# Optimization experiments

Measured on AMD Instinct MI355X. Metric: run time of the kernel, lower is better.

The kernel has to match this reference:

```python
import jax, jax.numpy as jnp
import numpy as np

B, T, D = 2, 2048, 2048
NH, NKV, HD = 16, 4, 128
ROPE_DIMS = 64
EPS = 1e-6


def _rope_tables(t, rd, base=10000.0):
    # rd dims are rotated as two halves of size rd//2; cos/sin are [T, rd]
    inv_freq = 1.0 / (base ** (jnp.arange(0, rd // 2, dtype=jnp.float32) * 2.0 / rd))
    ang = jnp.arange(t, dtype=jnp.float32)[:, None] * inv_freq[None, :]  # [T, rd//2]
    ang = jnp.concatenate([ang, ang], axis=-1)  # [T, rd]
    return jnp.cos(ang), jnp.sin(ang)


def setup_inputs() -> dict:
    key = jax.random.key(0)
    ks = jax.random.split(key, 6)
    x = jax.random.normal(ks[0], (B, T, D), dtype=jnp.float32)
    cos, sin = _rope_tables(T, ROPE_DIMS)
    s = 1.0 / np.sqrt(D)
    wq = jax.random.normal(ks[1], (NH * HD, D), dtype=jnp.float32) * s
    wk = jax.random.normal(ks[2], (NKV * HD, D), dtype=jnp.float32) * s
    wv = jax.random.normal(ks[3], (NKV * HD, D), dtype=jnp.float32) * s
    wo = jax.random.normal(ks[4], (NH * HD, D), dtype=jnp.float32).T * s  # [NH*HD, D] -> stored torch-style below
    wo = jax.random.normal(ks[5], (D, NH * HD), dtype=jnp.float32) * s  # torch Linear weight [out,in]
    w_norm = jnp.ones((D,), dtype=jnp.float32)
    return {"x": x, "cos": cos, "sin": sin, "w_norm": w_norm, "wq": wq,
            "wk": wk, "wv": wv, "wo": wo, "rope_dims": ROPE_DIMS, "use_xsa": 1}


def _rmsnorm(x, w, eps=EPS):
    ms = jnp.mean(x * x, axis=-1, keepdims=True)
    return x * jax.lax.rsqrt(ms + eps) * w


def _rotate_half(x):
    x1, x2 = jnp.split(x, 2, axis=-1)
    return jnp.concatenate([-x2, x1], axis=-1)


def _apply_partial_rope(q, k, cos, sin, rd):
    # q: [B,T,NH,HD], k: [B,T,NKV,HD]; cos/sin: [T,rd]
    c = cos[None, :, None, :]
    s = sin[None, :, None, :]
    def rot(t):
        tr, tp = t[..., :rd], t[..., rd:]
        tr = tr * c + _rotate_half(tr) * s
        return jnp.concatenate([tr, tp], axis=-1)
    return rot(q), rot(k)


def reference(x, cos, sin, w_norm, wq, wk, wv, wo, rope_dims, use_xsa):
    b, t, d = x.shape
    group = NH // NKV
    h = _rmsnorm(x, w_norm)
    q = jnp.einsum('btd,ed->bte', h, wq).reshape(b, t, NH, HD)
    k = jnp.einsum('btd,ed->bte', h, wk).reshape(b, t, NKV, HD)
    v = jnp.einsum('btd,ed->bte', h, wv).reshape(b, t, NKV, HD)
    q, k = _apply_partial_rope(q, k, cos, sin, rope_dims)
    # GQA: repeat KV heads across groups, then [B,H,T,HD]
    k = jnp.repeat(k, group, axis=2).transpose(0, 2, 1, 3)
    v = jnp.repeat(v, group, axis=2).transpose(0, 2, 1, 3)
    q = q.transpose(0, 2, 1, 3)
    scores = jnp.einsum('bhqd,bhkd->bhqk', q, k) / np.sqrt(HD)
    causal = jnp.tril(jnp.ones((t, t), dtype=bool))
    scores = jnp.where(causal[None, None], scores, jnp.finfo(scores.dtype).min)
    attn = jax.nn.softmax(scores, axis=-1)
    out = jnp.einsum('bhqk,bhkd->bhqd', attn, v)
    if use_xsa:
        dot = jnp.sum(out * v, axis=-1, keepdims=True)
        vns = jnp.sum(v * v, axis=-1, keepdims=True) + 1e-6
        out = out - dot * v / vns
    out = out.transpose(0, 2, 1, 3).reshape(b, t, NH * HD)
    return jnp.einsum('bte,de->btd', out, wo)
```

## Files before the change

### kernel.cpp

```cpp
#include <hip/hip_runtime.h>
#include <hip/hip_bf16.h>
#include <stdint.h>

#define B_ 2
#define T_ 2048
#define D_ 2048
#define NH_ 16
#define NKV_ 4
#define HD_ 128
#define EQ_ (NH_*HD_)
#define EKV_ (NKV_*HD_)
#define EQKV_ (EQ_ + 2*EKV_)
#define KOFF_ EQ_
#define VOFF_ (EQ_ + EKV_)

typedef __attribute__((ext_vector_type(8))) short short8;
typedef __attribute__((ext_vector_type(4))) short short4x;
typedef __attribute__((ext_vector_type(4))) float floatx4;

static __device__ __forceinline__ ushort f2bf(float f) {
  uint u = __builtin_bit_cast(uint, f);
  u = (u + 0x7fffu + ((u >> 16) & 1u)) >> 16;
  return (ushort)u;
}
static __device__ __forceinline__ float bf2f(ushort u) {
  return __builtin_bit_cast(float, ((uint)u) << 16);
}

#define S1_ (EQ_*D_)
#define S2_ (S1_ + EKV_*D_)
#define S3_ (S2_ + EKV_*D_)
#define S4_ (S3_ + D_*EQ_)
__global__ __launch_bounds__(256) void cvt4_k(const float* __restrict__ wq,
                                              const float* __restrict__ wk,
                                              const float* __restrict__ wv,
                                              const float* __restrict__ wo,
                                              ushort* __restrict__ wqkv,
                                              ushort* __restrict__ wob) {
  int i = (blockIdx.x * 256 + threadIdx.x) * 2;
  const float* s;
  ushort* d;
  int j;
  if (i < S1_)      { s = wq; d = wqkv + i; j = i; }
  else if (i < S2_) { s = wk; d = wqkv + i; j = i - S1_; }
  else if (i < S3_) { s = wv; d = wqkv + i; j = i - S2_; }
  else              { s = wo; d = wob + (i - S3_); j = i - S3_; }
  float2 f = *(const float2*)&s[j];
  ushort2 u;
  u.x = f2bf(f.x);
  u.y = f2bf(f.y);
  *(ushort2*)d = u;
}

__global__ __launch_bounds__(256) void rmsnorm_k(const float* __restrict__ x,
                                                 const float* __restrict__ wn,
                                                 ushort* __restrict__ hb) {
  const int row = blockIdx.x, tid = threadIdx.x;
  const int w = tid >> 6, lane = tid & 63;
  const float* xr = x + (size_t)row * D_;
  float v[8];
  float4 a = *(const float4*)&xr[tid * 8];
  float4 b = *(const float4*)&xr[tid * 8 + 4];
  v[0] = a.x; v[1] = a.y; v[2] = a.z; v[3] = a.w;
  v[4] = b.x; v[5] = b.y; v[6] = b.z; v[7] = b.w;
  float ss = 0.f;
#pragma unroll
  for (int i = 0; i < 8; i++) ss += v[i] * v[i];
  for (int m = 32; m; m >>= 1) ss += __shfl_xor(ss, m);
  __shared__ float red[4];
  if (lane == 0) red[w] = ss;
  __syncthreads();
  float tot = red[0] + red[1] + red[2] + red[3];
  float sc = rsqrtf(tot * (1.f / D_) + 1e-6f);
  short8 st;
#pragma unroll
  for (int i = 0; i < 8; i++) st[i] = (short)f2bf(v[i] * sc * wn[tid * 8 + i]);
  *(short8*)(hb + (size_t)row * D_ + tid * 8) = st;
}

template <bool OUT_F32>
__global__ __launch_bounds__(256) void gemm_bt(const ushort* __restrict__ A,
                                               const ushort* __restrict__ W,
                                               void* __restrict__ Cp,
                                               int M, int N, int K) {
  __shared__ __align__(16) ushort lA[128 * 64];
  __shared__ __align__(16) ushort lB[128 * 64];
  const int tid = threadIdx.x;
  const int w = tid >> 6, lane = tid & 63;
  const int bm = blockIdx.y, bn = blockIdx.x;
  const int wm = w >> 1, wn = w & 1;
  const int l15 = lane & 15, l4 = lane >> 4;
  const int swz = (l15 & 7) * 8;

  floatx4 acc[4][4];
#pragma unroll
  for (int m = 0; m < 4; m++)
#pragma unroll
    for (int n = 0; n < 4; n++) acc[m][n] = floatx4{0.f, 0.f, 0.f, 0.f};

  for (int k0 = 0; k0 < K; k0 += 64) {
#pragma unroll
    for (int r = 0; r < 4; ++r) {
      int c = r * 256 + tid;
      int row = c >> 3, cw = c & 7;
      int scol = k0 + ((cw ^ (row & 7)) << 3);
      const ushort* ga = A + (size_t)(bm * 128 + row) * K + scol;
      __builtin_amdgcn_global_load_lds(
          (const __attribute__((address_space(1))) void*)ga,
          (__attribute__((address_space(3))) void*)&lA[c * 8], 16, 0, 0);
      const ushort* gb = W + (size_t)(bn * 128 + row) * K + scol;
      __builtin_amdgcn_global_load_lds(
          (const __attribute__((address_space(1))) void*)gb,
          (__attribute__((address_space(3))) void*)&lB[c * 8], 16, 0, 0);
    }
    __syncthreads();
#pragma unroll
    for (int kk = 0; kk < 2; kk++) {
      short8 av[4], bv[4];
      int co = (kk * 32 + l4 * 8) ^ swz;
#pragma unroll
      for (int m = 0; m < 4; m++)
        av[m] = *(const short8*)&lA[(wm * 64 + m * 16 + l15) * 64 + co];
#pragma unroll
      for (int n = 0; n < 4; n++)
        bv[n] = *(const short8*)&lB[(wn * 64 + n * 16 + l15) * 64 + co];
#pragma unroll
      for (int m = 0; m < 4; m++)
#pragma unroll
        for (int n = 0; n < 4; n++)
          acc[m][n] = __builtin_amdgcn_mfma_f32_16x16x32_bf16(av[m], bv[n], acc[m][n], 0, 0, 0);
    }
    __syncthreads();
  }

  if (OUT_F32) {
    float* C = (float*)Cp;
#pragma unroll
    for (int m = 0; m < 4; m++)
#pragma unroll
      for (int n = 0; n < 4; n++)
#pragma unroll
        for (int j = 0; j < 4; j++) {
          int row = bm * 128 + wm * 64 + m * 16 + l4 * 4 + j;
          int col = bn * 128 + wn * 64 + n * 16 + l15;
          C[(size_t)row * N + col] = acc[m][n][j];
        }
  } else {
    ushort* C = (ushort*)Cp;
#pragma unroll
    for (int m = 0; m < 4; m++)
#pragma unroll
      for (int n = 0; n < 4; n++)
#pragma unroll
        for (int j = 0; j < 4; j++) {
          int row = bm * 128 + wm * 64 + m * 16 + l4 * 4 + j;
          int col = bn * 128 + wn * 64 + n * 16 + l15;
          C[(size_t)row * N + col] = f2bf(acc[m][n][j]);
        }
  }
}

__global__ __launch_bounds__(256) void rope_k(ushort* __restrict__ X,
                                              const float* __restrict__ cosT,
                                              const float* __restrict__ sinT,
                                              int rd) {
  int idx = blockIdx.x * 256 + threadIdx.x;
  int half = rd >> 1;
  int total = B_ * T_ * (NH_ + NKV_) * half;
  if (idx >= total) return;
  int i = idx % half;
  int r2 = idx / half;
  int hh = r2 % (NH_ + NKV_);
  int row = r2 / (NH_ + NKV_);
  int t = row % T_;
  int col = (hh < NH_) ? hh * HD_ : KOFF_ + (hh - NH_) * HD_;
  ushort* p = X + (size_t)row * EQKV_ + col;
  float x0 = bf2f(p[i]), x1 = bf2f(p[i + half]);
  float c0 = cosT[t * rd + i], s0 = sinT[t * rd + i];
  float c1 = cosT[t * rd + i + half], s1 = sinT[t * rd + i + half];
  p[i] = f2bf(x0 * c0 - x1 * s0);
  p[i + half] = f2bf(x1 * c1 + x0 * s1);
}

__global__ __launch_bounds__(256) void vtr_k(const ushort* __restrict__ V,
                                             int vstride,
                                             ushort* __restrict__ Vt) {
  __shared__ ushort tile[32][34];
  const int tb = blockIdx.x, eb = blockIdx.y, b = blockIdx.z;
  const int tid = threadIdx.x;
  const int r = tid >> 3, c4 = (tid & 7) * 4;
  short4x in = *(const short4x*)&V[((size_t)(b * T_ + tb * 32 + r)) * vstride + eb * 32 + c4];
#pragma unroll
  for (int i = 0; i < 4; i++) tile[r][c4 + i] = (ushort)in[i];
  __syncthreads();
  short4x out;
#pragma unroll
  for (int i = 0; i < 4; i++) out[i] = (short)tile[c4 + i][r];
  *(short4x*)&Vt[((size_t)(b * EKV_ + eb * 32 + r)) * T_ + tb * 32 + c4] = out;
}

__global__ __launch_bounds__(256, 2) void attn_k(const ushort* __restrict__ QKV,
                                                 const ushort* __restrict__ Vt,
                                                 const int* __restrict__ flag,
                                                 ushort* __restrict__ att) {
  __shared__ __align__(16) ushort Klds[2][8192];
  __shared__ __align__(16) ushort Vlds[2][8192];
  __shared__ __align__(16) char P_lds[4 * 2048];
  const int tid = threadIdx.x, w = tid >> 6, lane = tid & 63;
  const int l15 = lane & 15, l4 = lane >> 4;
  const int h = blockIdx.y, b = blockIdx.z, kv = h >> 2;
  const int px = blockIdx.x;
  const int wbase = w * 2048;
  const float c_ = 0.12752626f;
  const float THR_ = 90.5f;
  const int flagv = *flag;

  const ushort* Kh = QKV + KOFF_ + (size_t)b * T_ * EQKV_ + kv * HD_;
  const ushort* Vth = Vt + ((size_t)(b * EKV_ + kv * HD_)) * T_;

  auto stageK = [&](int buf, const ushort* kp) {
#pragma unroll
    for (int i = 0; i < 4; i++) {
      int q = i * 256 + tid;
      int r = q >> 4, cw = q & 15;
      const ushort* src = kp + (size_t)r * EQKV_ + ((cw ^ (r & 7)) << 3);
      __builtin_amdgcn_global_load_lds(
          (const __attribute__((address_space(1))) void*)src,
          (__attribute__((address_space(3))) void*)&Klds[buf][q * 8], 16, 0, 0);
    }
  };
  auto stageV = [&](int buf, const ushort* vp) {
#pragma unroll
    for (int i = 0; i < 4; i++) {
      int q = i * 256 + tid;
      int d = q >> 3, cw = q & 7;
      const ushort* src = vp + (size_t)d * T_ + ((cw ^ (d & 7)) << 3);
      __builtin_amdgcn_global_load_lds(
          (const __attribute__((address_space(1))) void*)src,
          (__attribute__((address_space(3))) void*)&Vlds[buf][q * 8], 16, 0, 0);
    }
  };

  for (int hh = 0; hh < 2; hh++) {
    const int qb = hh ? (31 - px) : px;
    const int nt = qb + 1;
    const int qbase = qb * 64 + w * 16;

    short8 qf[4];
#pragma unroll
    for (int kk = 0; kk < 4; kk++)
      qf[kk] = *(const short8*)&QKV[(size_t)(b * T_ + qbase + l15) * EQKV_ + h * HD_ + kk * 32 + l4 * 8];

    floatx4 acc_o[8];
#pragma unroll
    for (int nn = 0; nn < 8; nn++) acc_o[nn] = floatx4{0.f, 0.f, 0.f, 0.f};
    float mj[4] = {-1e30f, -1e30f, -1e30f, -1e30f};
    float lj[4] = {0.f, 0.f, 0.f, 0.f};

    const ushort* kp = Kh;
    const ushort* vp = Vth;
    stageV(0, vp);
    stageK(0, kp);
    __syncthreads();
    int cur = 0;

    for (int t = 0; t < nt; t++) {
      if (t + 1 < nt) {
        stageV(cur ^ 1, vp + 64);
        stageK(cur ^ 1, kp + 64 * EQKV_);
      }
      kp += 64 * EQKV_;
      vp += 64;

      floatx4 s[4];
#pragma unroll
      for (int n = 0; n < 4; n++) s[n] = floatx4{0.f, 0.f, 0.f, 0.f};
      __builtin_amdgcn_s_setprio(1);
#pragma unroll
      for (int n = 0; n < 4; n++) {
        int row = n * 16 + l15;
#pragma unroll
        for (int kk = 0; kk < 4; kk++) {
          int bc = (kk * 64 + l4 * 16) ^ ((row & 7) << 4);
          short8 kf = *(const short8*)&Klds[cur][row * 128 + (bc >> 1)];
          s[n] = __builtin_amdgcn_mfma_f32_16x16x32_bf16(qf[kk], kf, s[n], 0, 0, 0);
        }
      }
      __builtin_amdgcn_s_setprio(0);

      float pm[4] = {-1e30f, -1e30f, -1e30f, -1e30f};
      if (t == nt - 1) {
#pragma unroll
        for (int n = 0; n < 4; n++)
#pragma unroll
          for (int j = 0; j < 4; j++) {
            int col = (nt - 1) * 64 + n * 16 + l15;
            int row = qbase + l4 * 4 + j;
            float sv = (col <= row) ? s[n][j] : -1e30f;
            s[n][j] = sv;
            pm[j] = fmaxf(pm[j], sv);
          }
      } else {
#pragma unroll
        for (int n = 0; n < 4; n++)
#pragma unroll
          for (int j = 0; j < 4; j++) pm[j] = fmaxf(pm[j], s[n][j]);
      }
#pragma unroll
      for (int j = 0; j < 4; j++) {
        pm[j] = fmaxf(pm[j], __shfl_xor(pm[j], 1));
        pm[j] = fmaxf(pm[j], __shfl_xor(pm[j], 2));
        pm[j] = fmaxf(pm[j], __shfl_xor(pm[j], 4));
        pm[j] = fmaxf(pm[j], __shfl_xor(pm[j], 8));
      }
      float worst = fmaxf(fmaxf(pm[0] - mj[0], pm[1] - mj[1]),
                          fmaxf(pm[2] - mj[2], pm[3] - mj[3]));
      if (!__all(worst <= THR_)) {
#pragma unroll
        for (int j = 0; j < 4; j++) {
          float mn = fmaxf(mj[j], pm[j]);
          float sc = exp2f((mj[j] - mn) * c_);
          mj[j] = mn;
          lj[j] *= sc;
#pragma unroll
          for (int nn = 0; nn < 8; nn++) acc_o[nn][j] *= sc;
        }
      }
      float mc[4];
#pragma unroll
      for (int j = 0; j < 4; j++) mc[j] = mj[j] * c_;
      float ps[4] = {0.f, 0.f, 0.f, 0.f};
#pragma unroll
      for (int n = 0; n < 4; n++)
#pragma unroll
        for (int j = 0; j < 4; j++) {
          float p = exp2f(__builtin_fmaf(s[n][j], c_, -mc[j]));
          ps[j] += p;
          uint pu = (__builtin_bit_cast(uint, p) + 0x8000u) >> 16;
          int r = l4 * 4 + j;
          int byteoff = ((r * 128 + (n * 16 + l15) * 2) ^ ((r & 7) << 4));
          *(ushort*)(P_lds + wbase + byteoff) = (ushort)pu;
        }

      __builtin_amdgcn_s_setprio(1);
#pragma unroll
      for (int kk = 0; kk < 2; kk++) {
        int rbyte = ((l15 * 128 + kk * 64 + l4 * 16) ^ ((l15 & 7) << 4));
        short8 pa = *(const short8*)(P_lds + wbase + rbyte);
#pragma unroll
        for (int n = 0; n < 8; n++) {
          int d = n * 16 + l15;
          int bc = (kk * 64 + l4 * 16) ^ ((d & 7) << 4);
          short8 vf = *(const short8*)&Vlds[cur][d * 64 + (bc >> 1)];
          acc_o[n] = __builtin_amdgcn_mfma_f32_16x16x32_bf16(pa, vf, acc_o[n], 0, 0, 0);
        }
      }
      __builtin_amdgcn_s_setprio(0);
#pragma unroll
      for (int j = 0; j < 4; j++) {
        ps[j] += __shfl_xor(ps[j], 1);
        ps[j] += __shfl_xor(ps[j], 2);
        ps[j] += __shfl_xor(ps[j], 4);
        ps[j] += __shfl_xor(ps[j], 8);
        lj[j] += ps[j];
      }
      __syncthreads();
      cur ^= 1;
    }

#pragma unroll
    for (int j = 0; j < 4; j++) {
      float inv = 1.f / lj[j];
      int q = qbase + l4 * 4 + j;
      const ushort* vq = QKV + VOFF_ + (size_t)(b * T_ + q) * EQKV_ + kv * HD_;
      float ov[8], vv[8], dot = 0.f, vns = 0.f;
#pragma unroll
      for (int n = 0; n < 8; n++) {
        float o = acc_o[n][j] * inv;
        float v = bf2f(vq[n * 16 + l15]);
        ov[n] = o;
        vv[n] = v;
        dot += o * v;
        vns += v * v;
      }
      dot += __shfl_xor(dot, 1); vns += __shfl_xor(vns, 1);
      dot += __shfl_xor(dot, 2); vns += __shfl_xor(vns, 2);
      dot += __shfl_xor(dot, 4); vns += __shfl_xor(vns, 4);
      dot += __shfl_xor(dot, 8); vns += __shfl_xor(vns, 8);
      if (flagv) {
        float f = dot / (vns + 1e-6f);
#pragma unroll
        for (int n = 0; n < 8; n++) ov[n] -= f * vv[n];
      }
      ushort* ap = att + (size_t)(b * T_ + q) * EQ_ + h * HD_;
#pragma unroll
      for (int n = 0; n < 8; n++) ap[n * 16 + l15] = f2bf(ov[n]);
    }
  }
}

extern "C" void kernel_launch(void* const* d_in, const int* in_sizes, int n_in,
                              void* d_out, int out_size, void* d_ws, size_t ws_size,
                              hipStream_t stream) {
  const float* x    = (const float*)d_in[0];
  const float* cosT = (const float*)d_in[1];
  const float* sinT = (const float*)d_in[2];
  const float* wn   = (const float*)d_in[3];
  const float* wq   = (const float*)d_in[4];
  const float* wk   = (const float*)d_in[5];
  const float* wv   = (const float*)d_in[6];
  const float* wo   = (const float*)d_in[7];
  const int* use_xsa = (const int*)d_in[9];
  int rd = in_sizes[1] / T_;

  char* ws = (char*)d_ws;
  size_t off = 0;
  auto alloc = [&](size_t bytes) {
    char* p = ws + off;
    off += (bytes + 255) & ~(size_t)255;
    return p;
  };
  ushort* h_b    = (ushort*)alloc((size_t)B_ * T_ * D_ * 2);
  ushort* qkv_b  = (ushort*)alloc((size_t)B_ * T_ * EQKV_ * 2);
  ushort* wqkv_b = (ushort*)alloc((size_t)EQKV_ * D_ * 2);
  ushort* wo_b   = (ushort*)alloc((size_t)D_ * EQ_ * 2);
  ushort* att_b  = h_b;
  ushort* vt_b   = wqkv_b;

  cvt4_k<<<S4_ / 512, 256, 0, stream>>>(wq, wk, wv, wo, wqkv_b, wo_b);
  rmsnorm_k<<<B_ * T_, 256, 0, stream>>>(x, wn, h_b);

  dim3 gqkv(EQKV_ / 128, B_ * T_ / 128);
  gemm_bt<false><<<gqkv, 256, 0, stream>>>(h_b, wqkv_b, qkv_b, B_ * T_, EQKV_, D_);

  dim3 gvt(T_ / 32, EKV_ / 32, B_);
  vtr_k<<<gvt, 256, 0, stream>>>(qkv_b + VOFF_, EQKV_, vt_b);

  int half = rd / 2;
  int tot = B_ * T_ * (NH_ + NKV_) * half;
  rope_k<<<(tot + 255) / 256, 256, 0, stream>>>(qkv_b, cosT, sinT, rd);

  dim3 ga(16, NH_, B_);
  attn_k<<<ga, 256, 0, stream>>>(qkv_b, vt_b, use_xsa, att_b);

  dim3 go(D_ / 128, B_ * T_ / 128);
  gemm_bt<true><<<go, 256, 0, stream>>>(att_b, wo_b, d_out, B_ * T_, D_, D_);
}
```

Measured before the change: 225.1 us.

## Load V fragments directly from global memory and raise attention occupancy

The attention kernel no longer stages transposed V tiles into double-buffered LDS. Each wave now reads its V fragments straight from global memory (via cache) inside the PV loop, and the launch bound is raised from 2 to 4 blocks per CU. Dropping the V buffers cuts LDS use so more blocks can fit on a CU, trading shared staging for redundant per-wave global loads with latency exposed right before the MFMAs. The tighter register budget from the higher launch bound may force spills.

```diff
diff --git a/kernel.cpp b/kernel.cpp
--- a/kernel.cpp
+++ b/kernel.cpp
@@ -199,12 +199,11 @@
   *(short4x*)&Vt[((size_t)(b * EKV_ + eb * 32 + r)) * T_ + tb * 32 + c4] = out;
 }
 
-__global__ __launch_bounds__(256, 2) void attn_k(const ushort* __restrict__ QKV,
+__global__ __launch_bounds__(256, 4) void attn_k(const ushort* __restrict__ QKV,
                                                  const ushort* __restrict__ Vt,
                                                  const int* __restrict__ flag,
                                                  ushort* __restrict__ att) {
   __shared__ __align__(16) ushort Klds[2][8192];
-  __shared__ __align__(16) ushort Vlds[2][8192];
   __shared__ __align__(16) char P_lds[4 * 2048];
   const int tid = threadIdx.x, w = tid >> 6, lane = tid & 63;
   const int l15 = lane & 15, l4 = lane >> 4;
@@ -229,17 +228,6 @@
           (__attribute__((address_space(3))) void*)&Klds[buf][q * 8], 16, 0, 0);
     }
   };
-  auto stageV = [&](int buf, const ushort* vp) {
-#pragma unroll
-    for (int i = 0; i < 4; i++) {
-      int q = i * 256 + tid;
-      int d = q >> 3, cw = q & 7;
-      const ushort* src = vp + (size_t)d * T_ + ((cw ^ (d & 7)) << 3);
-      __builtin_amdgcn_global_load_lds(
-          (const __attribute__((address_space(1))) void*)src,
-          (__attribute__((address_space(3))) void*)&Vlds[buf][q * 8], 16, 0, 0);
-    }
-  };
 
   for (int hh = 0; hh < 2; hh++) {
     const int qb = hh ? (31 - px) : px;
@@ -258,19 +246,15 @@
     float lj[4] = {0.f, 0.f, 0.f, 0.f};
 
     const ushort* kp = Kh;
-    const ushort* vp = Vth;
-    stageV(0, vp);
     stageK(0, kp);
     __syncthreads();
     int cur = 0;
 
     for (int t = 0; t < nt; t++) {
-      if (t + 1 < nt) {
-        stageV(cur ^ 1, vp + 64);
+      const int kvb = t * 64;
+      if (t + 1 < nt)
         stageK(cur ^ 1, kp + 64 * EQKV_);
-      }
       kp += 64 * EQKV_;
-      vp += 64;
 
       floatx4 s[4];
 #pragma unroll
@@ -345,15 +329,15 @@
       __builtin_amdgcn_s_setprio(1);
 #pragma unroll
       for (int kk = 0; kk < 2; kk++) {
+        short8 vf[8];
+#pragma unroll
+        for (int n = 0; n < 8; n++)
+          vf[n] = *(const short8*)&Vth[(size_t)(n * 16 + l15) * T_ + kvb + kk * 32 + l4 * 8];
         int rbyte = ((l15 * 128 + kk * 64 + l4 * 16) ^ ((l15 & 7) << 4));
         short8 pa = *(const short8*)(P_lds + wbase + rbyte);
 #pragma unroll
-        for (int n = 0; n < 8; n++) {
-          int d = n * 16 + l15;
-          int bc = (kk * 64 + l4 * 16) ^ ((d & 7) << 4);
-          short8 vf = *(const short8*)&Vlds[cur][d * 64 + (bc >> 1)];
-          acc_o[n] = __builtin_amdgcn_mfma_f32_16x16x32_bf16(pa, vf, acc_o[n], 0, 0, 0);
-        }
+        for (int n = 0; n < 8; n++)
+          acc_o[n] = __builtin_amdgcn_mfma_f32_16x16x32_bf16(pa, vf[n], acc_o[n], 0, 0, 0);
       }
       __builtin_amdgcn_s_setprio(0);
 #pragma unroll
```

Result: slower. 353.8 us (+57.2%).

## Compute transposed S tile and feed P to PV MFMA via lane shuffles

Applied to the files above, without the earlier changes.

Swaps the QK^T MFMA operands so each lane holds scores for a single query row. Row max and sum then need only two cross-lane shuffles instead of sixteen, and online-softmax state becomes one scalar per lane. P is packed to bf16 with v_cvt_pk_bf16_f32 and rearranged into the PV A-operand layout with ds_bpermute shuffles, which removes the P staging buffer in LDS and its write/read round trip. In exchange it adds per-tile shuffles for the rescale factors and the P fragments, plus select logic.

```diff
diff --git a/kernel.cpp b/kernel.cpp
--- a/kernel.cpp
+++ b/kernel.cpp
@@ -17,6 +17,7 @@
 typedef __attribute__((ext_vector_type(8))) short short8;
 typedef __attribute__((ext_vector_type(4))) short short4x;
 typedef __attribute__((ext_vector_type(4))) float floatx4;
+typedef __attribute__((ext_vector_type(4))) uint uintx4;
 
 static __device__ __forceinline__ ushort f2bf(float f) {
   uint u = __builtin_bit_cast(uint, f);
@@ -25,6 +26,11 @@
 }
 static __device__ __forceinline__ float bf2f(ushort u) {
   return __builtin_bit_cast(float, ((uint)u) << 16);
+}
+static __device__ __forceinline__ uint cvt_pk_bf16(float lo, float hi) {
+  uint r;
+  asm("v_cvt_pk_bf16_f32 %0, %1, %2" : "=v"(r) : "v"(lo), "v"(hi));
+  return r;
 }
 
 #define S1_ (EQ_*D_)
@@ -205,12 +211,13 @@
                                                  ushort* __restrict__ att) {
   __shared__ __align__(16) ushort Klds[2][8192];
   __shared__ __align__(16) ushort Vlds[2][8192];
-  __shared__ __align__(16) char P_lds[4 * 2048];
   const int tid = threadIdx.x, w = tid >> 6, lane = tid & 63;
   const int l15 = lane & 15, l4 = lane >> 4;
+  const int alpha = lane >> 5;
+  const int srcA = ((lane >> 4) & 1) * 32 + l15;
+  const int srcB = srcA + 16;
   const int h = blockIdx.y, b = blockIdx.z, kv = h >> 2;
   const int px = blockIdx.x;
-  const int wbase = w * 2048;
   const float c_ = 0.12752626f;
   const float THR_ = 90.5f;
   const int flagv = *flag;
@@ -245,6 +252,7 @@
     const int qb = hh ? (31 - px) : px;
     const int nt = qb + 1;
     const int qbase = qb * 64 + w * 16;
+    const int myq = qbase + l15;
 
     short8 qf[4];
 #pragma unroll
@@ -254,8 +262,8 @@
     floatx4 acc_o[8];
 #pragma unroll
     for (int nn = 0; nn < 8; nn++) acc_o[nn] = floatx4{0.f, 0.f, 0.f, 0.f};
-    float mj[4] = {-1e30f, -1e30f, -1e30f, -1e30f};
-    float lj[4] = {0.f, 0.f, 0.f, 0.f};
+    float m_ = -1e30f;
+    float l_ = 0.f;
 
     const ushort* kp = Kh;
     const ushort* vp = Vth;
@@ -265,6 +273,7 @@
     int cur = 0;
 
     for (int t = 0; t < nt; t++) {
+      const int kvb = t * 64;
       if (t + 1 < nt) {
         stageV(cur ^ 1, vp + 64);
         stageK(cur ^ 1, kp + 64 * EQKV_);
@@ -283,70 +292,87 @@
         for (int kk = 0; kk < 4; kk++) {
           int bc = (kk * 64 + l4 * 16) ^ ((row & 7) << 4);
           short8 kf = *(const short8*)&Klds[cur][row * 128 + (bc >> 1)];
-          s[n] = __builtin_amdgcn_mfma_f32_16x16x32_bf16(qf[kk], kf, s[n], 0, 0, 0);
+          s[n] = __builtin_amdgcn_mfma_f32_16x16x32_bf16(kf, qf[kk], s[n], 0, 0, 0);
         }
       }
       __builtin_amdgcn_s_setprio(0);
 
-      float pm[4] = {-1e30f, -1e30f, -1e30f, -1e30f};
+      float pm = -1e30f;
       if (t == nt - 1) {
 #pragma unroll
         for (int n = 0; n < 4; n++)
 #pragma unroll
           for (int j = 0; j < 4; j++) {
-            int col = (nt - 1) * 64 + n * 16 + l15;
-            int row = qbase + l4 * 4 + j;
-            float sv = (col <= row) ? s[n][j] : -1e30f;
+            int k = kvb + n * 16 + l4 * 4 + j;
+            float sv = (k <= myq) ? s[n][j] : -1e30f;
             s[n][j] = sv;
-            pm[j] = fmaxf(pm[j], sv);
+            pm = fmaxf(pm, sv);
           }
       } else {
 #pragma unroll
         for (int n = 0; n < 4; n++)
 #pragma unroll
-          for (int j = 0; j < 4; j++) pm[j] = fmaxf(pm[j], s[n][j]);
-      }
-#pragma unroll
-      for (int j = 0; j < 4; j++) {
-        pm[j] = fmaxf(pm[j], __shfl_xor(pm[j], 1));
-        pm[j] = fmaxf(pm[j], __shfl_xor(pm[j], 2));
-        pm[j] = fmaxf(pm[j], __shfl_xor(pm[j], 4));
-        pm[j] = fmaxf(pm[j], __shfl_xor(pm[j], 8));
-      }
-      float worst = fmaxf(fmaxf(pm[0] - mj[0], pm[1] - mj[1]),
-                          fmaxf(pm[2] - mj[2], pm[3] - mj[3]));
-      if (!__all(worst <= THR_)) {
+          for (int j = 0; j < 4; j++) pm = fmaxf(pm, s[n][j]);
+      }
+      pm = fmaxf(pm, __shfl_xor(pm, 16));
+      pm = fmaxf(pm, __shfl_xor(pm, 32));
+
+      if (!__all(pm - m_ <= THR_)) {
+        float mn = fmaxf(m_, pm);
+        float f = exp2f((m_ - mn) * c_);
+        m_ = mn;
+        l_ *= f;
+        float fj0 = __shfl(f, l4 * 4 + 0);
+        float fj1 = __shfl(f, l4 * 4 + 1);
+        float fj2 = __shfl(f, l4 * 4 + 2);
+        float fj3 = __shfl(f, l4 * 4 + 3);
+#pragma unroll
+        for (int nn = 0; nn < 8; nn++) {
+          acc_o[nn][0] *= fj0;
+          acc_o[nn][1] *= fj1;
+          acc_o[nn][2] *= fj2;
+          acc_o[nn][3] *= fj3;
+        }
+      }
+
+      float mc = m_ * c_;
+      float ps = 0.f;
+      float p_[4][4];
+#pragma unroll
+      for (int n = 0; n < 4; n++)
 #pragma unroll
         for (int j = 0; j < 4; j++) {
-          float mn = fmaxf(mj[j], pm[j]);
-          float sc = exp2f((mj[j] - mn) * c_);
-          mj[j] = mn;
-          lj[j] *= sc;
-#pragma unroll
-          for (int nn = 0; nn < 8; nn++) acc_o[nn][j] *= sc;
-        }
-      }
-      float mc[4];
-#pragma unroll
-      for (int j = 0; j < 4; j++) mc[j] = mj[j] * c_;
-      float ps[4] = {0.f, 0.f, 0.f, 0.f};
-#pragma unroll
-      for (int n = 0; n < 4; n++)
-#pragma unroll
-        for (int j = 0; j < 4; j++) {
-          float p = exp2f(__builtin_fmaf(s[n][j], c_, -mc[j]));
-          ps[j] += p;
-          uint pu = (__builtin_bit_cast(uint, p) + 0x8000u) >> 16;
-          int r = l4 * 4 + j;
-          int byteoff = ((r * 128 + (n * 16 + l15) * 2) ^ ((r & 7) << 4));
-          *(ushort*)(P_lds + wbase + byteoff) = (ushort)pu;
-        }
+          float p = exp2f(__builtin_fmaf(s[n][j], c_, -mc));
+          p_[n][j] = p;
+          ps += p;
+        }
+      ps += __shfl_xor(ps, 16);
+      ps += __shfl_xor(ps, 32);
+      l_ += ps;
+      uint pk01[4], pk23[4];
+#pragma unroll
+      for (int n = 0; n < 4; n++) {
+        pk01[n] = cvt_pk_bf16(p_[n][0], p_[n][1]);
+        pk23[n] = cvt_pk_bf16(p_[n][2], p_[n][3]);
+      }
 
       __builtin_amdgcn_s_setprio(1);
 #pragma unroll
       for (int kk = 0; kk < 2; kk++) {
-        int rbyte = ((l15 * 128 + kk * 64 + l4 * 16) ^ ((l15 & 7) << 4));
-        short8 pa = *(const short8*)(P_lds + wbase + rbyte);
+        int a01_0 = __shfl((int)pk01[2 * kk + 0], srcA);
+        int a01_1 = __shfl((int)pk01[2 * kk + 1], srcA);
+        int a23_0 = __shfl((int)pk23[2 * kk + 0], srcA);
+        int a23_1 = __shfl((int)pk23[2 * kk + 1], srcA);
+        int b01_0 = __shfl((int)pk01[2 * kk + 0], srcB);
+        int b01_1 = __shfl((int)pk01[2 * kk + 1], srcB);
+        int b23_0 = __shfl((int)pk23[2 * kk + 0], srcB);
+        int b23_1 = __shfl((int)pk23[2 * kk + 1], srcB);
+        uintx4 du;
+        du.x = (uint)(alpha ? a01_1 : a01_0);
+        du.y = (uint)(alpha ? a23_1 : a23_0);
+        du.z = (uint)(alpha ? b01_1 : b01_0);
+        du.w = (uint)(alpha ? b23_1 : b23_0);
+        short8 pa = __builtin_bit_cast(short8, du);
 #pragma unroll
         for (int n = 0; n < 8; n++) {
           int d = n * 16 + l15;
@@ -356,21 +382,14 @@
         }
       }
       __builtin_amdgcn_s_setprio(0);
-#pragma unroll
-      for (int j = 0; j < 4; j++) {
-        ps[j] += __shfl_xor(ps[j], 1);
-        ps[j] += __shfl_xor(ps[j], 2);
-        ps[j] += __shfl_xor(ps[j], 4);
-        ps[j] += __shfl_xor(ps[j], 8);
-        lj[j] += ps[j];
-      }
       __syncthreads();
       cur ^= 1;
     }
 
+    float inv_ = 1.f / l_;
 #pragma unroll
     for (int j = 0; j < 4; j++) {
-      float inv = 1.f / lj[j];
+      float inv = __shfl(inv_, l4 * 4 + j);
       int q = qbase + l4 * 4 + j;
       const ushort* vq = QKV + VOFF_ + (size_t)(b * T_ + q) * EQKV_ + kv * HD_;
       float ov[8], vv[8], dot = 0.f, vns = 0.f;
```

Result: faster. 211.9 us (-5.9%).
